# Kernel optimization log

Hardware: AMD Instinct MI355X
Metric: run time of the kernel (lower is better)

Reference implementation:

```python
import jax, jax.numpy as jnp
import numpy as np

D_MODEL = 1024
NUM_HEADS = 16
D_K = D_MODEL // NUM_HEADS


def setup_inputs() -> dict:
    key = jax.random.key(0)
    ks = jax.random.split(key, 11)
    B, S = 2, 2048
    scale = 1.0 / np.sqrt(D_MODEL)
    inp = {
        "Q_in": jax.random.normal(ks[0], (B, S, D_MODEL), jnp.float32),
        "K_in": jax.random.normal(ks[1], (B, S, D_MODEL), jnp.float32),
        "V_in": jax.random.normal(ks[2], (B, S, D_MODEL), jnp.float32),
        "Wq": jax.random.normal(ks[3], (D_MODEL, D_MODEL), jnp.float32) * scale,
        "bq": jnp.zeros((D_MODEL,), jnp.float32),
        "Wk": jax.random.normal(ks[4], (D_MODEL, D_MODEL), jnp.float32) * scale,
        "bk": jnp.zeros((D_MODEL,), jnp.float32),
        "Wv": jax.random.normal(ks[5], (D_MODEL, D_MODEL), jnp.float32) * scale,
        "bv": jnp.zeros((D_MODEL,), jnp.float32),
        "Wfc": jax.random.normal(ks[6], (D_MODEL, D_MODEL), jnp.float32) * scale,
        "bfc": jnp.zeros((D_MODEL,), jnp.float32),
    }
    return inp


def _split_heads(x, B):
    # [B, S, D] -> [B, H, S, d_k]
    return x.reshape(B, -1, NUM_HEADS, D_K).transpose(0, 2, 1, 3)


def reference(Q_in, K_in, V_in, Wq, bq, Wk, bk, Wv, bv, Wfc, bfc):
    B = Q_in.shape[0]
    q = _split_heads(Q_in @ Wq + bq, B)
    k = _split_heads(K_in @ Wk + bk, B)
    v = _split_heads(V_in @ Wv + bv, B)
    # scaled dot-product attention (mask=None)
    scores = jnp.einsum("bhqd,bhkd->bhqk", q, k) / jnp.sqrt(jnp.float32(D_K))
    attn = jax.nn.softmax(scores, axis=-1)
    ctx = jnp.einsum("bhqk,bhkd->bhqd", attn, v)
    out = ctx.transpose(0, 2, 1, 3).reshape(B, -1, D_MODEL)
    out = out @ Wfc + bfc
    return out, attn
```

## Files before the change

kernel.cpp:

```cpp
#include <hip/hip_runtime.h>

typedef unsigned short u16;
typedef _Float16 f16;
typedef __attribute__((ext_vector_type(8))) f16 f16x8;
typedef __attribute__((ext_vector_type(4))) float f32x4;
typedef __attribute__((ext_vector_type(4))) u16 u16x4;
typedef __attribute__((ext_vector_type(8))) u16 u16x8;

__device__ __forceinline__ u16 f2h(float x){
  f16 h = (f16)x;
  return __builtin_bit_cast(u16, h);
}
__device__ __forceinline__ float h2f(u16 v){
  return (float)__builtin_bit_cast(f16, v);
}

__device__ __forceinline__ void stage16(const void* g, void* l){
  __builtin_amdgcn_global_load_lds(
      (const __attribute__((address_space(1))) unsigned*)g,
      (__attribute__((address_space(3))) unsigned*)l, 16, 0, 0);
}

__global__ __launch_bounds__(256) void convert_x3(
    const float* __restrict__ in0, const float* __restrict__ in1, const float* __restrict__ in2,
    u16* __restrict__ o0, u16* __restrict__ o1, u16* __restrict__ o2){
  const int b = blockIdx.x >> 12;
  const int i = (blockIdx.x & 4095) * 256 + threadIdx.x;
  const float* in = (b == 0) ? in0 : (b == 1) ? in1 : in2;
  u16* out = (b == 0) ? o0 : (b == 1) ? o1 : o2;
  f32x4 v = ((const f32x4*)in)[i];
  u16x4 h;
  #pragma unroll
  for (int j = 0; j < 4; j++) h[j] = f2h(v[j]);
  ((u16x4*)out)[i] = h;
}

__global__ __launch_bounds__(256) void transpose_w4(
    const float* __restrict__ W0, const float* __restrict__ W1,
    const float* __restrict__ W2, const float* __restrict__ W3,
    u16* __restrict__ t0, u16* __restrict__ t1, u16* __restrict__ t2, u16* __restrict__ t3){
  __shared__ float tile[64][68];
  const int z = blockIdx.z;
  const float* W = (z == 0) ? W0 : (z == 1) ? W1 : (z == 2) ? W2 : W3;
  u16* wt = (z == 0) ? t0 : (z == 1) ? t1 : (z == 2) ? t2 : t3;
  const int tid = threadIdx.x;
  const int k0 = blockIdx.y * 64, n0 = blockIdx.x * 64;
  #pragma unroll
  for (int g = 0; g < 4; g++){
    int flat4 = g * 256 + tid;
    int row = flat4 >> 4, c4 = flat4 & 15;
    f32x4 v = *(const f32x4*)&W[(size_t)(k0 + row) * 1024 + n0 + c4 * 4];
    *(f32x4*)&tile[row][c4 * 4] = v;
  }
  __syncthreads();
  const int n = tid >> 2, kc = (tid & 3) * 16;
  u16x8 o0, o1;
  #pragma unroll
  for (int j = 0; j < 8; j++){
    o0[j] = f2h(tile[kc + j][n]);
    o1[j] = f2h(tile[kc + 8 + j][n]);
  }
  u16* dst = &wt[(size_t)(n0 + n) * 1024 + k0 + kc];
  *(u16x8*)dst = o0;
  *(u16x8*)(dst + 8) = o1;
}

template<int MODE>
__device__ __forceinline__ void gemm_body(
    const u16* __restrict__ A, const u16* __restrict__ B,
    const float* __restrict__ bias,
    float* __restrict__ outF, u16* __restrict__ outH,
    int N, int K, int bx, int by)
{
  __shared__ u16 sA[128 * 32];
  __shared__ u16 sB[128 * 32];
  const int tid = threadIdx.x;
  const int wid = tid >> 6, lane = tid & 63;
  const int lm = lane & 15, lg = lane >> 4;
  const int bm = by * 128, bn = bx * 128;
  const int wrow = (wid >> 1) * 64, wcol = (wid & 1) * 64;
  const int srow = tid >> 2;
  const int skc  = (tid & 3) * 8;

  f32x4 acc[4][4] = {};

  for (int kt = 0; kt < K; kt += 32){
    {
      char* dA = (char*)sA + wid * 1024;
      char* dB = (char*)sB + wid * 1024;
      stage16(A + (size_t)(bm +      srow) * K + kt + skc, dA);
      stage16(A + (size_t)(bm + 64 + srow) * K + kt + skc, dA + 4096);
      stage16(B + (size_t)(bn +      srow) * K + kt + skc, dB);
      stage16(B + (size_t)(bn + 64 + srow) * K + kt + skc, dB + 4096);
    }
    __syncthreads();
    f16x8 af[4], bf[4];
    #pragma unroll
    for (int mf = 0; mf < 4; mf++)
      af[mf] = *(const f16x8*)&sA[(wrow + mf * 16 + lm) * 32 + lg * 8];
    #pragma unroll
    for (int nf = 0; nf < 4; nf++)
      bf[nf] = *(const f16x8*)&sB[(wcol + nf * 16 + lm) * 32 + lg * 8];
    #pragma unroll
    for (int mf = 0; mf < 4; mf++)
      #pragma unroll
      for (int nf = 0; nf < 4; nf++)
        acc[mf][nf] = __builtin_amdgcn_mfma_f32_16x16x32_f16(af[mf], bf[nf], acc[mf][nf], 0, 0, 0);
    __syncthreads();
  }

  #pragma unroll
  for (int mf = 0; mf < 4; mf++)
    #pragma unroll
    for (int nf = 0; nf < 4; nf++){
      const int n  = bn + wcol + nf * 16 + lm;
      const int mb = bm + wrow + mf * 16 + lg * 4;
      #pragma unroll
      for (int r = 0; r < 4; r++){
        const int m = mb + r;
        float v = acc[mf][nf][r] + ((MODE == 2) ? bias[m] : bias[n]);
        if constexpr (MODE == 0){
          outF[(size_t)m * N + n] = v;
        } else if constexpr (MODE == 1){
          const size_t idx = (((size_t)((m >> 11) * 16 + (n >> 6))) * 2048 + (m & 2047)) * 64 + (n & 63);
          outH[idx] = f2h(v);
        } else {
          const size_t idx = (((size_t)((n >> 11) * 16 + (m >> 6))) * 64 + (m & 63)) * 2048 + (n & 2047);
          outH[idx] = f2h(v);
        }
      }
    }
}

__global__ __launch_bounds__(256, 2) void gemm_qkv(
    const u16* __restrict__ xq, const u16* __restrict__ wqt, const float* __restrict__ bq, u16* __restrict__ qh,
    const u16* __restrict__ xk, const u16* __restrict__ wkt, const float* __restrict__ bk, u16* __restrict__ kh,
    const u16* __restrict__ wvt, const u16* __restrict__ xv, const float* __restrict__ bv, u16* __restrict__ vt){
  const int z = blockIdx.z;
  if (z == 2){
    gemm_body<2>(wvt, xv, bv, nullptr, vt, 4096, 1024, blockIdx.y, blockIdx.x);
  } else if (z == 1){
    gemm_body<1>(xk, wkt, bk, nullptr, kh, 1024, 1024, blockIdx.x, blockIdx.y);
  } else {
    gemm_body<1>(xq, wqt, bq, nullptr, qh, 1024, 1024, blockIdx.x, blockIdx.y);
  }
}

__global__ __launch_bounds__(256, 2) void gemm_fc(
    const u16* __restrict__ ctx, const u16* __restrict__ wft, const float* __restrict__ bfc, float* __restrict__ outF){
  gemm_body<0>(ctx, wft, bfc, outF, nullptr, 1024, 1024, blockIdx.x, blockIdx.y);
}

#define MFMA16(A, B, C) __builtin_amdgcn_mfma_f32_16x16x32_f16((A), (B), (C), 0, 0, 0)

__global__ __launch_bounds__(256, 2) void attn_fused(
    const u16* __restrict__ qh_, const u16* __restrict__ kh_,
    const u16* __restrict__ vt_,
    float* __restrict__ attn_out, u16* __restrict__ ctx)
{
  constexpr int S = 2048;
  __shared__ __align__(16) char smem[4 * 16640];
  __shared__ float sred[4][16];
  __shared__ float linv[16];
  const int tid = threadIdx.x, wid = tid >> 6, lane = tid & 63;
  const int lm = lane & 15, lg = lane >> 4;
  u16 (*pb)[520] = (u16 (*)[520])(smem + wid * 16640);
  float (*credw)[20] = (float (*)[20])(smem + wid * 16640);

  const int wg = blockIdx.x;
  const int xcd = wg & 7, li = wg >> 3;
  const int bh = (xcd << 2) + (li >> 7);
  const int q0 = (li & 127) * 16;
  const size_t base = (size_t)bh * S * 64;
  const u16* Qh = qh_ + base;
  const u16* Kh = kh_ + base;
  const u16* Vt = vt_ + base;
  float* Aout = attn_out + (size_t)bh * S * S;
  const int kbase = wid * 512;
  const int b = bh >> 4, h = bh & 15;
  const float SCL2 = 0.18033688011112042f;

  const u16* qp = Qh + (size_t)(q0 + lm) * 64 + lg * 8;
  f16x8 qb0 = *(const f16x8*)(qp);
  f16x8 qb1 = *(const f16x8*)(qp + 32);

  f16x8 vs[3][4], ks4[3][4];
  #define LOADF(nt2_, s_) do {                                              \
    const int col0_ = kbase + (nt2_) * 32;                                  \
    _Pragma("unroll")                                                       \
    for (int nf_ = 0; nf_ < 4; nf_++)                                       \
      vs[s_][nf_] = *(const f16x8*)(Vt + (size_t)(nf_ * 16 + lm) * S + col0_ + lg * 8); \
    const u16* kp_ = Kh + (size_t)(col0_ + lm) * 64 + lg * 8;               \
    ks4[s_][0] = *(const f16x8*)(kp_);                                      \
    ks4[s_][1] = *(const f16x8*)(kp_ + 32);                                 \
    ks4[s_][2] = *(const f16x8*)(kp_ + 1024);                               \
    ks4[s_][3] = *(const f16x8*)(kp_ + 1024 + 32);                          \
  } while (0)

  LOADF(0, 0);
  LOADF(1, 1);

  float part = 0.0f;
  f32x4 cacc[4] = {};
  #pragma unroll
  for (int nt2 = 0; nt2 < 16; ++nt2){
    if (nt2 < 14) LOADF(nt2 + 2, (nt2 + 2) % 3);
    const int cs = nt2 % 3;
    f32x4 c0 = {}, c1 = {};
    c0 = MFMA16(ks4[cs][0], qb0, c0);
    c0 = MFMA16(ks4[cs][1], qb1, c0);
    c1 = MFMA16(ks4[cs][2], qb0, c1);
    c1 = MFMA16(ks4[cs][3], qb1, c1);
    u16x4 hp0, hp1;
    #pragma unroll
    for (int r = 0; r < 4; r++){
      float e = __builtin_amdgcn_exp2f(c0[r] * SCL2);
      part += e; hp0[r] = f2h(e);
    }
    #pragma unroll
    for (int r = 0; r < 4; r++){
      float e = __builtin_amdgcn_exp2f(c1[r] * SCL2);
      part += e; hp1[r] = f2h(e);
    }
    *(u16x4*)&pb[lm][nt2 * 32 + lg * 4] = hp0;
    *(u16x4*)&pb[lm][nt2 * 32 + 16 + lg * 4] = hp1;
    f16x8 pa = *(const f16x8*)&pb[lm][nt2 * 32 + lg * 8];
    #pragma unroll
    for (int nf = 0; nf < 4; nf++)
      cacc[nf] = MFMA16(pa, vs[cs][nf], cacc[nf]);
  }
  #undef LOADF

  part += __shfl_xor(part, 16);
  part += __shfl_xor(part, 32);
  if (lane < 16) sred[wid][lm] = part;
  __syncthreads();
  if (tid < 16) linv[tid] = 1.0f / (sred[0][tid] + sred[1][tid] + sred[2][tid] + sred[3][tid]);
  __syncthreads();

  #pragma unroll 2
  for (int r = 0; r < 16; r++){
    const float iv = linv[r];
    float* rowp = Aout + (size_t)(q0 + r) * S + kbase;
    #pragma unroll
    for (int ch = 0; ch < 2; ch++){
      u16x4 hv = *(const u16x4*)&pb[r][ch * 256 + lane * 4];
      f32x4 av = { h2f(hv[0]) * iv, h2f(hv[1]) * iv, h2f(hv[2]) * iv, h2f(hv[3]) * iv };
      *(f32x4*)(rowp + ch * 256 + lane * 4) = av;
    }
  }

  __syncthreads();

  float iv4[4];
  #pragma unroll
  for (int r = 0; r < 4; r++) iv4[r] = linv[lg * 4 + r];
  #pragma unroll
  for (int nf = 0; nf < 4; nf++){
    f32x4 sc;
    #pragma unroll
    for (int r = 0; r < 4; r++) sc[r] = cacc[nf][r] * iv4[r];
    *(f32x4*)&credw[nf * 16 + lm][lg * 4] = sc;
  }
  __syncthreads();
  {
    const float (*cr0)[20] = (const float (*)[20])(smem + 0 * 16640);
    const float (*cr1)[20] = (const float (*)[20])(smem + 1 * 16640);
    const float (*cr2)[20] = (const float (*)[20])(smem + 2 * 16640);
    const float (*cr3)[20] = (const float (*)[20])(smem + 3 * 16640);
    const int rd = lane, rq = wid * 4;
    f32x4 s0 = *(const f32x4*)&cr0[rd][rq];
    f32x4 s1 = *(const f32x4*)&cr1[rd][rq];
    f32x4 s2 = *(const f32x4*)&cr2[rd][rq];
    f32x4 s3 = *(const f32x4*)&cr3[rd][rq];
    #pragma unroll
    for (int j = 0; j < 4; j++){
      float v = s0[j] + s1[j] + s2[j] + s3[j];
      ctx[(size_t)(b * 2048 + q0 + rq + j) * 1024 + h * 64 + rd] = f2h(v);
    }
  }
}

extern "C" void kernel_launch(void* const* d_in, const int* in_sizes, int n_in,
                              void* d_out, int out_size, void* d_ws, size_t ws_size,
                              hipStream_t stream) {
  const float* Qi  = (const float*)d_in[0];
  const float* Ki  = (const float*)d_in[1];
  const float* Vi  = (const float*)d_in[2];
  const float* Wq  = (const float*)d_in[3];
  const float* bq  = (const float*)d_in[4];
  const float* Wk  = (const float*)d_in[5];
  const float* bk  = (const float*)d_in[6];
  const float* Wv  = (const float*)d_in[7];
  const float* bv  = (const float*)d_in[8];
  const float* Wfc = (const float*)d_in[9];
  const float* bfc = (const float*)d_in[10];

  char* w = (char*)d_ws;
  const size_t P  = 8388608;
  const size_t PW = 2097152;
  u16* xq  = (u16*)(w + 0*P);
  u16* xk  = (u16*)(w + 1*P);
  u16* xv  = (u16*)(w + 2*P);
  u16* qh  = (u16*)(w + 3*P);
  u16* kh  = (u16*)(w + 4*P);
  u16* vt  = (u16*)(w + 5*P);
  u16* ctx = (u16*)(w + 6*P);
  char* w2 = w + 7*P;
  u16* wqt = (u16*)(w2 + 0*PW);
  u16* wkt = (u16*)(w2 + 1*PW);
  u16* wvt = (u16*)(w2 + 2*PW);
  u16* wft = (u16*)(w2 + 3*PW);

  float* outp  = (float*)d_out;
  float* attnp = outp + 4194304;

  convert_x3<<<12288, 256, 0, stream>>>(Qi, Ki, Vi, xq, xk, xv);
  transpose_w4<<<dim3(16, 16, 4), 256, 0, stream>>>(Wq, Wk, Wv, Wfc, wqt, wkt, wvt, wft);

  gemm_qkv<<<dim3(8, 32, 3), 256, 0, stream>>>(xq, wqt, bq, qh,
                                               xk, wkt, bk, kh,
                                               wvt, xv, bv, vt);
  attn_fused<<<4096, 256, 0, stream>>>(qh, kh, vt, attnp, ctx);
  gemm_fc<<<dim3(8, 32), 256, 0, stream>>>(ctx, wft, bfc, outp);
}
```

Before: 366.4 us.

## Split attention into a row-sum pass and a normalized pass to shrink LDS

The fused attention kernel now runs two passes. The first pass computes only the softmax row sums from QK^T, loading just K. The second pass recomputes the scores, writes already-normalized probabilities and accumulates P·V, storing the fp32 attention matrix every half-tile of 256 columns. This halves the per-wave probability buffer in shared memory, so launch bounds can go from 2 to 4 blocks per CU, aiming for more occupancy to overlap the large attention-matrix stores. The cost is recomputing the QK^T MFMAs and exponentials and reading K twice.

```diff
diff --git a/kernel.cpp b/kernel.cpp
--- a/kernel.cpp
+++ b/kernel.cpp
@@ -153,19 +153,19 @@
 
 #define MFMA16(A, B, C) __builtin_amdgcn_mfma_f32_16x16x32_f16((A), (B), (C), 0, 0, 0)
 
-__global__ __launch_bounds__(256, 2) void attn_fused(
+__global__ __launch_bounds__(256, 4) void attn_fused(
     const u16* __restrict__ qh_, const u16* __restrict__ kh_,
     const u16* __restrict__ vt_,
     float* __restrict__ attn_out, u16* __restrict__ ctx)
 {
   constexpr int S = 2048;
-  __shared__ __align__(16) char smem[4 * 16640];
+  __shared__ __align__(16) char smem[4 * 8448];
   __shared__ float sred[4][16];
   __shared__ float linv[16];
   const int tid = threadIdx.x, wid = tid >> 6, lane = tid & 63;
   const int lm = lane & 15, lg = lane >> 4;
-  u16 (*pb)[520] = (u16 (*)[520])(smem + wid * 16640);
-  float (*credw)[20] = (float (*)[20])(smem + wid * 16640);
+  u16 (*pb)[264] = (u16 (*)[264])(smem + wid * 8448);
+  float (*credw)[20] = (float (*)[20])(smem + wid * 8448);
 
   const int wg = blockIdx.x;
   const int xcd = wg & 7, li = wg >> 3;
@@ -184,90 +184,105 @@
   f16x8 qb0 = *(const f16x8*)(qp);
   f16x8 qb1 = *(const f16x8*)(qp + 32);
 
-  f16x8 vs[3][4], ks4[3][4];
-  #define LOADF(nt2_, s_) do {                                              \
-    const int col0_ = kbase + (nt2_) * 32;                                  \
-    _Pragma("unroll")                                                       \
-    for (int nf_ = 0; nf_ < 4; nf_++)                                       \
-      vs[s_][nf_] = *(const f16x8*)(Vt + (size_t)(nf_ * 16 + lm) * S + col0_ + lg * 8); \
-    const u16* kp_ = Kh + (size_t)(col0_ + lm) * 64 + lg * 8;               \
-    ks4[s_][0] = *(const f16x8*)(kp_);                                      \
-    ks4[s_][1] = *(const f16x8*)(kp_ + 32);                                 \
-    ks4[s_][2] = *(const f16x8*)(kp_ + 1024);                               \
-    ks4[s_][3] = *(const f16x8*)(kp_ + 1024 + 32);                          \
-  } while (0)
-
-  LOADF(0, 0);
-  LOADF(1, 1);
-
-  float part = 0.0f;
+  {
+    f16x8 ka[3][4];
+    #define LOADK(nt2_, s_) do {                                            \
+      const u16* kp_ = Kh + (size_t)(kbase + (nt2_) * 32 + lm) * 64 + lg * 8; \
+      ka[s_][0] = *(const f16x8*)(kp_);                                     \
+      ka[s_][1] = *(const f16x8*)(kp_ + 32);                                \
+      ka[s_][2] = *(const f16x8*)(kp_ + 1024);                              \
+      ka[s_][3] = *(const f16x8*)(kp_ + 1024 + 32);                         \
+    } while (0)
+    LOADK(0, 0);
+    LOADK(1, 1);
+    float part = 0.0f;
+    #pragma unroll
+    for (int nt2 = 0; nt2 < 16; ++nt2){
+      if (nt2 < 14) LOADK(nt2 + 2, (nt2 + 2) % 3);
+      const int cs = nt2 % 3;
+      f32x4 c0 = {}, c1 = {};
+      c0 = MFMA16(ka[cs][0], qb0, c0);
+      c0 = MFMA16(ka[cs][1], qb1, c0);
+      c1 = MFMA16(ka[cs][2], qb0, c1);
+      c1 = MFMA16(ka[cs][3], qb1, c1);
+      #pragma unroll
+      for (int r = 0; r < 4; r++){
+        part += __builtin_amdgcn_exp2f(c0[r] * SCL2);
+        part += __builtin_amdgcn_exp2f(c1[r] * SCL2);
+      }
+    }
+    #undef LOADK
+    part += __shfl_xor(part, 16);
+    part += __shfl_xor(part, 32);
+    if (lane < 16) sred[wid][lm] = part;
+  }
+  __syncthreads();
+  if (tid < 16) linv[tid] = 1.0f / (sred[0][tid] + sred[1][tid] + sred[2][tid] + sred[3][tid]);
+  __syncthreads();
+  const float inv = linv[lm];
+
   f32x4 cacc[4] = {};
-  #pragma unroll
-  for (int nt2 = 0; nt2 < 16; ++nt2){
-    if (nt2 < 14) LOADF(nt2 + 2, (nt2 + 2) % 3);
-    const int cs = nt2 % 3;
-    f32x4 c0 = {}, c1 = {};
-    c0 = MFMA16(ks4[cs][0], qb0, c0);
-    c0 = MFMA16(ks4[cs][1], qb1, c0);
-    c1 = MFMA16(ks4[cs][2], qb0, c1);
-    c1 = MFMA16(ks4[cs][3], qb1, c1);
-    u16x4 hp0, hp1;
-    #pragma unroll
-    for (int r = 0; r < 4; r++){
-      float e = __builtin_amdgcn_exp2f(c0[r] * SCL2);
-      part += e; hp0[r] = f2h(e);
-    }
-    #pragma unroll
-    for (int r = 0; r < 4; r++){
-      float e = __builtin_amdgcn_exp2f(c1[r] * SCL2);
-      part += e; hp1[r] = f2h(e);
-    }
-    *(u16x4*)&pb[lm][nt2 * 32 + lg * 4] = hp0;
-    *(u16x4*)&pb[lm][nt2 * 32 + 16 + lg * 4] = hp1;
-    f16x8 pa = *(const f16x8*)&pb[lm][nt2 * 32 + lg * 8];
-    #pragma unroll
-    for (int nf = 0; nf < 4; nf++)
-      cacc[nf] = MFMA16(pa, vs[cs][nf], cacc[nf]);
-  }
-  #undef LOADF
-
-  part += __shfl_xor(part, 16);
-  part += __shfl_xor(part, 32);
-  if (lane < 16) sred[wid][lm] = part;
-  __syncthreads();
-  if (tid < 16) linv[tid] = 1.0f / (sred[0][tid] + sred[1][tid] + sred[2][tid] + sred[3][tid]);
-  __syncthreads();
-
-  #pragma unroll 2
-  for (int r = 0; r < 16; r++){
-    const float iv = linv[r];
-    float* rowp = Aout + (size_t)(q0 + r) * S + kbase;
-    #pragma unroll
-    for (int ch = 0; ch < 2; ch++){
-      u16x4 hv = *(const u16x4*)&pb[r][ch * 256 + lane * 4];
-      f32x4 av = { h2f(hv[0]) * iv, h2f(hv[1]) * iv, h2f(hv[2]) * iv, h2f(hv[3]) * iv };
-      *(f32x4*)(rowp + ch * 256 + lane * 4) = av;
-    }
-  }
-
-  __syncthreads();
-
-  float iv4[4];
-  #pragma unroll
-  for (int r = 0; r < 4; r++) iv4[r] = linv[lg * 4 + r];
-  #pragma unroll
-  for (int nf = 0; nf < 4; nf++){
-    f32x4 sc;
-    #pragma unroll
-    for (int r = 0; r < 4; r++) sc[r] = cacc[nf][r] * iv4[r];
-    *(f32x4*)&credw[nf * 16 + lm][lg * 4] = sc;
-  }
-  __syncthreads();
   {
-    const float (*cr0)[20] = (const float (*)[20])(smem + 0 * 16640);
-    const float (*cr1)[20] = (const float (*)[20])(smem + 1 * 16640);
-    const float (*cr2)[20] = (const float (*)[20])(smem + 2 * 16640);
-    const float (*cr3)[20] = (const float (*)[20])(smem + 3 * 16640);
+    f16x8 kb2[2][4], vb2[2][4];
+    #define LOADKV(nt2_, s_) do {                                           \
+      const int col0_ = kbase + (nt2_) * 32;                                \
+      _Pragma("unroll")                                                     \
+      for (int nf_ = 0; nf_ < 4; nf_++)                                     \
+        vb2[s_][nf_] = *(const f16x8*)(Vt + (size_t)(nf_ * 16 + lm) * S + col0_ + lg * 8); \
+      const u16* kp_ = Kh + (size_t)(col0_ + lm) * 64 + lg * 8;             \
+      kb2[s_][0] = *(const f16x8*)(kp_);                                    \
+      kb2[s_][1] = *(const f16x8*)(kp_ + 32);                               \
+      kb2[s_][2] = *(const f16x8*)(kp_ + 1024);                             \
+      kb2[s_][3] = *(const f16x8*)(kp_ + 1024 + 32);                        \
+    } while (0)
+    LOADKV(0, 0);
+    #pragma unroll
+    for (int half = 0; half < 2; ++half){
+      #pragma unroll
+      for (int j = 0; j < 8; ++j){
+        const int nt2 = half * 8 + j;
+        if (nt2 < 15) LOADKV(nt2 + 1, (nt2 + 1) & 1);
+        const int cs = nt2 & 1;
+        f32x4 c0 = {}, c1 = {};
+        c0 = MFMA16(kb2[cs][0], qb0, c0);
+        c0 = MFMA16(kb2[cs][1], qb1, c0);
+        c1 = MFMA16(kb2[cs][2], qb0, c1);
+        c1 = MFMA16(kb2[cs][3], qb1, c1);
+        u16x4 hp0, hp1;
+        #pragma unroll
+        for (int r = 0; r < 4; r++)
+          hp0[r] = f2h(__builtin_amdgcn_exp2f(c0[r] * SCL2) * inv);
+        #pragma unroll
+        for (int r = 0; r < 4; r++)
+          hp1[r] = f2h(__builtin_amdgcn_exp2f(c1[r] * SCL2) * inv);
+        *(u16x4*)&pb[lm][j * 32 + lg * 4] = hp0;
+        *(u16x4*)&pb[lm][j * 32 + 16 + lg * 4] = hp1;
+        f16x8 pa = *(const f16x8*)&pb[lm][j * 32 + lg * 8];
+        #pragma unroll
+        for (int nf = 0; nf < 4; nf++)
+          cacc[nf] = MFMA16(pa, vb2[cs][nf], cacc[nf]);
+      }
+      #pragma unroll 2
+      for (int r = 0; r < 16; r++){
+        u16x4 hv = *(const u16x4*)&pb[r][lane * 4];
+        f32x4 av = { h2f(hv[0]), h2f(hv[1]), h2f(hv[2]), h2f(hv[3]) };
+        *(f32x4*)(Aout + (size_t)(q0 + r) * S + kbase + half * 256 + lane * 4) = av;
+      }
+    }
+    #undef LOADKV
+  }
+
+  __syncthreads();
+
+  #pragma unroll
+  for (int nf = 0; nf < 4; nf++)
+    *(f32x4*)&credw[nf * 16 + lm][lg * 4] = cacc[nf];
+  __syncthreads();
+  {
+    const float (*cr0)[20] = (const float (*)[20])(smem + 0 * 8448);
+    const float (*cr1)[20] = (const float (*)[20])(smem + 1 * 8448);
+    const float (*cr2)[20] = (const float (*)[20])(smem + 2 * 8448);
+    const float (*cr3)[20] = (const float (*)[20])(smem + 3 * 8448);
     const int rd = lane, rq = wid * 4;
     f32x4 s0 = *(const f32x4*)&cr0[rd][rq];
     f32x4 s1 = *(const f32x4*)&cr1[rd][rq];
```

Measured after the change: 468.5 us. 1.28x slower.
